# Kernel tuning notes

Measured on AMD Instinct MI355X. Metric: run time of the kernel, lower is better.

## Reference

```python
import jax, jax.numpy as jnp
import numpy as np

B, N, DIM = 1, 32768, 512
HEADS, DIM_HEAD, AGENT_NUM = 8, 64, 256
INNER = HEADS * DIM_HEAD  # 512 == DIM
SCALE = DIM_HEAD ** -0.5


def setup_inputs() -> dict:
    key = jax.random.key(0)
    ks = jax.random.split(key, 9)
    s = lambda fan: 1.0 / np.sqrt(fan)
    return {
        "x": jax.random.normal(ks[0], (B, N, DIM), dtype=jnp.float32),
        "W_qkv": jax.random.normal(ks[1], (3 * INNER, DIM), dtype=jnp.float32) * s(DIM),
        "agent": jax.random.normal(ks[2], (HEADS, AGENT_NUM, DIM_HEAD), dtype=jnp.float32),
        "W_noise": jax.random.normal(ks[3], (DIM_HEAD, DIM_HEAD), dtype=jnp.float32) * s(DIM_HEAD),
        "b_noise": jax.random.normal(ks[4], (DIM_HEAD,), dtype=jnp.float32) * s(DIM_HEAD),
        "W_mask": jax.random.normal(ks[5], (DIM_HEAD, DIM_HEAD), dtype=jnp.float32) * s(DIM_HEAD),
        "b_mask": jax.random.normal(ks[6], (DIM_HEAD,), dtype=jnp.float32) * s(DIM_HEAD),
        "W_thresh": jax.random.normal(ks[7], (1, DIM), dtype=jnp.float32) * s(DIM),
        "b_thresh": jax.random.normal(ks[8], (1,), dtype=jnp.float32) * s(DIM),
    }


def reference(x, W_qkv, agent, W_noise, b_noise, W_mask, b_mask, W_thresh, b_thresh):
    b, n, _ = x.shape
    h, d, a = HEADS, DIM_HEAD, AGENT_NUM
    # qkv projection (no bias), split and reshape to b h n d
    qkv = x @ W_qkv.T                                  # [b, n, 3*h*d]
    q, k, v = jnp.split(qkv, 3, axis=-1)
    tohd = lambda t: t.reshape(b, n, h, d).transpose(0, 2, 1, 3)  # [b,h,n,d]
    q, k, v = tohd(q), tohd(k), tohd(v)
    # agent attention: q attends to agents, agents attend to k
    q_attn = jax.nn.softmax(jnp.einsum('bhnd,had->bhna', q, agent) * SCALE, axis=-1)  # [b,h,n,a]
    k_attn = jax.nn.softmax(jnp.einsum('had,bhnd->bhan', agent, k), axis=-1)          # [b,h,a,n]
    kv = jnp.einsum('bhan,bhnd->bhad', k_attn, v)      # [b,h,a,d]
    # threshold from pooled kv (classical): Linear(dim,1) -> mean -> sigmoid
    kv_c = kv.reshape(b, a, h * d)                     # row-major reshape, same as torch
    thresh = jax.nn.sigmoid(jnp.mean(kv_c @ W_thresh.T + b_thresh))
    # noise / mask gating
    noise = jax.nn.sigmoid(kv @ W_noise.T + b_noise)
    mask_v = jax.nn.sigmoid(kv @ W_mask.T + b_mask)
    mask_b = jnp.where(mask_v > thresh, 1.0, 0.0).astype(kv.dtype)
    kv = kv * mask_b + noise                           # tem == 0
    kv = jax.nn.softmax(kv, axis=-1)
    out = jnp.einsum('bhna,bhad->bhnd', q_attn, kv)    # [b,h,n,d]
    return out.transpose(0, 2, 1, 3).reshape(b, n, h * d)
```

## Files before the change

### kernel.cpp

```cpp
#include <hip/hip_runtime.h>
#include <hip/hip_bf16.h>
#include <math.h>

#define N_TOK 32768
#define DIMX 512
#define HEADS 8
#define DHEAD 64
#define ANUM 256
#define SCALE_Q 0.125f
#define KVCHUNK 1024
#define NCHUNK 32
#define STRIP 8192

typedef __bf16 v8bf __attribute__((ext_vector_type(8)));
typedef float v4f __attribute__((ext_vector_type(4)));
typedef unsigned short u16x8 __attribute__((ext_vector_type(8)));

typedef __attribute__((address_space(1))) const void gas_void;
typedef __attribute__((address_space(3))) void las_void;

__device__ __forceinline__ void gld16(const void* g, void* l) {
    __builtin_amdgcn_global_load_lds((gas_void*)g, (las_void*)l, 16, 0, 0);
}

__device__ inline unsigned short f2bf(float f) {
    unsigned u = __float_as_uint(f);
    return (unsigned short)((u + 0x7fffu + ((u >> 16) & 1u)) >> 16);
}
__device__ inline float bf2f(unsigned short s) {
    return __uint_as_float((unsigned)s << 16);
}

__global__ __launch_bounds__(256) void k_cvt3(const float* __restrict__ src,
                                              unsigned short* __restrict__ ph,
                                              unsigned short* __restrict__ pm,
                                              unsigned short* __restrict__ pl,
                                              int n8) {
    for (int i = blockIdx.x * 256 + threadIdx.x; i < n8; i += gridDim.x * 256) {
        float4 a = ((const float4*)src)[2 * i];
        float4 b = ((const float4*)src)[2 * i + 1];
        float v[8] = {a.x, a.y, a.z, a.w, b.x, b.y, b.z, b.w};
        u16x8 H, M, L;
        #pragma unroll
        for (int j = 0; j < 8; ++j) {
            unsigned short h = f2bf(v[j]);
            float r1 = v[j] - bf2f(h);
            unsigned short m = f2bf(r1);
            float r2 = r1 - bf2f(m);
            H[j] = h; M[j] = m; L[j] = f2bf(r2);
        }
        ((u16x8*)ph)[i] = H;
        ((u16x8*)pm)[i] = M;
        ((u16x8*)pl)[i] = L;
    }
}

__global__ __launch_bounds__(256, 2) void k_gemm(
        const unsigned short* __restrict__ xh, const unsigned short* __restrict__ xm,
        const unsigned short* __restrict__ xl,
        const unsigned short* __restrict__ wh, const unsigned short* __restrict__ wm,
        const unsigned short* __restrict__ wl,
        unsigned short* __restrict__ qb, float* __restrict__ kvb,
        unsigned short* __restrict__ vhg, unsigned short* __restrict__ vmg, int mbase) {
    __shared__ __align__(16) unsigned short lds[6 * 4096];
    unsigned short* Ah = lds;
    unsigned short* Am = lds + 4096;
    unsigned short* Al = lds + 8192;
    unsigned short* Bh = lds + 12288;
    unsigned short* Bm = lds + 16384;
    unsigned short* Bl = lds + 20480;
    const int tid = threadIdx.x;
    const int lane = tid & 63;
    const int wid = tid >> 6;
    const int wr = wid >> 1;
    const int wc = wid & 1;
    const int lin = blockIdx.x;
    const int swz = (lin & 7) * 96 + (lin >> 3);
    const int mloc0 = (swz / 12) * 128;
    const int j0 = (swz % 12) * 128;
    const bool isQ = (j0 < 512);
#define SWZ(row, ks) ((row) * 64 + (((ks) ^ (((row) >> 1) & 3)) << 4))
    const int srow0 = tid >> 2;
    const int srow1 = srow0 + 64;
    const int ksw = tid & 3;
    const int ks0 = ksw ^ ((srow0 >> 1) & 3);
    const int ks1 = ksw ^ ((srow1 >> 1) & 3);
    const size_t ga0 = (size_t)(mloc0 + srow0) * DIMX + ks0 * 8;
    const size_t ga1 = (size_t)(mloc0 + srow1) * DIMX + ks1 * 8;
    const size_t gb0 = (size_t)(j0 + srow0) * DIMX + ks0 * 8;
    const size_t gb1 = (size_t)(j0 + srow1) * DIMX + ks1 * 8;
    const int lo0 = tid * 16;
    const int lo1 = 4096 + tid * 16;

    v4f acc[4][4];
    #pragma unroll
    for (int i = 0; i < 4; ++i)
        #pragma unroll
        for (int j = 0; j < 4; ++j)
            #pragma unroll
            for (int r = 0; r < 4; ++r) acc[i][j][r] = 0.0f;

    const int fm = lane & 15;
    const int fks = lane >> 4;
    int aofs[4], bofs[4];
    #pragma unroll
    for (int i = 0; i < 4; ++i) {
        const int am = wr * 64 + i * 16 + fm;
        const int bm = wc * 64 + i * 16 + fm;
        aofs[i] = SWZ(am, fks);
        bofs[i] = SWZ(bm, fks);
    }
#undef SWZ

    for (int k0 = 0; k0 < DIMX; k0 += 32) {
        __syncthreads();
        gld16(xh + ga0 + k0, (char*)Ah + lo0);
        gld16(xh + ga1 + k0, (char*)Ah + lo1);
        gld16(xm + ga0 + k0, (char*)Am + lo0);
        gld16(xm + ga1 + k0, (char*)Am + lo1);
        gld16(wh + gb0 + k0, (char*)Bh + lo0);
        gld16(wh + gb1 + k0, (char*)Bh + lo1);
        gld16(wm + gb0 + k0, (char*)Bm + lo0);
        gld16(wm + gb1 + k0, (char*)Bm + lo1);
        if (!isQ) {
            gld16(xl + ga0 + k0, (char*)Al + lo0);
            gld16(xl + ga1 + k0, (char*)Al + lo1);
            gld16(wl + gb0 + k0, (char*)Bl + lo0);
            gld16(wl + gb1 + k0, (char*)Bl + lo1);
        }
        __syncthreads();
        v8bf fah[4], fbh[4];
        #pragma unroll
        for (int i = 0; i < 4; ++i) {
            fah[i] = *(const v8bf*)((const char*)Ah + aofs[i]);
            fbh[i] = *(const v8bf*)((const char*)Bh + bofs[i]);
        }
        #pragma unroll
        for (int mi = 0; mi < 4; ++mi)
            #pragma unroll
            for (int ni = 0; ni < 4; ++ni)
                acc[mi][ni] = __builtin_amdgcn_mfma_f32_16x16x32_bf16(fah[mi], fbh[ni], acc[mi][ni], 0, 0, 0);
        v8bf fam[4], fbm[4];
        #pragma unroll
        for (int i = 0; i < 4; ++i) {
            fam[i] = *(const v8bf*)((const char*)Am + aofs[i]);
            fbm[i] = *(const v8bf*)((const char*)Bm + bofs[i]);
        }
        #pragma unroll
        for (int mi = 0; mi < 4; ++mi)
            #pragma unroll
            for (int ni = 0; ni < 4; ++ni) {
                acc[mi][ni] = __builtin_amdgcn_mfma_f32_16x16x32_bf16(fah[mi], fbm[ni], acc[mi][ni], 0, 0, 0);
                acc[mi][ni] = __builtin_amdgcn_mfma_f32_16x16x32_bf16(fam[mi], fbh[ni], acc[mi][ni], 0, 0, 0);
            }
        if (!isQ) {
            #pragma unroll
            for (int mi = 0; mi < 4; ++mi)
                #pragma unroll
                for (int ni = 0; ni < 4; ++ni)
                    acc[mi][ni] = __builtin_amdgcn_mfma_f32_16x16x32_bf16(fam[mi], fbm[ni], acc[mi][ni], 0, 0, 0);
            v8bf fal[4], fbl[4];
            #pragma unroll
            for (int i = 0; i < 4; ++i) {
                fal[i] = *(const v8bf*)((const char*)Al + aofs[i]);
                fbl[i] = *(const v8bf*)((const char*)Bl + bofs[i]);
            }
            #pragma unroll
            for (int mi = 0; mi < 4; ++mi)
                #pragma unroll
                for (int ni = 0; ni < 4; ++ni) {
                    acc[mi][ni] = __builtin_amdgcn_mfma_f32_16x16x32_bf16(fah[mi], fbl[ni], acc[mi][ni], 0, 0, 0);
                    acc[mi][ni] = __builtin_amdgcn_mfma_f32_16x16x32_bf16(fal[mi], fbh[ni], acc[mi][ni], 0, 0, 0);
                }
        }
    }
    const int crow = (lane >> 4) * 4;
    const int ccol = lane & 15;
    if (isQ) {
        #pragma unroll
        for (int mi = 0; mi < 4; ++mi)
            #pragma unroll
            for (int ni = 0; ni < 4; ++ni) {
                const int j = j0 + wc * 64 + ni * 16 + ccol;
                #pragma unroll
                for (int r = 0; r < 4; ++r) {
                    const int m = mbase + mloc0 + wr * 64 + mi * 16 + crow + r;
                    qb[(size_t)m * DIMX + j] = f2bf(acc[mi][ni][r]);
                }
            }
    } else if (j0 < 1024) {
        #pragma unroll
        for (int mi = 0; mi < 4; ++mi)
            #pragma unroll
            for (int ni = 0; ni < 4; ++ni) {
                const int j = j0 - 512 + wc * 64 + ni * 16 + ccol;
                #pragma unroll
                for (int r = 0; r < 4; ++r) {
                    const int m = mbase + mloc0 + wr * 64 + mi * 16 + crow + r;
                    kvb[(size_t)m * 512 + j] = acc[mi][ni][r];
                }
            }
    } else {
        #pragma unroll
        for (int mi = 0; mi < 4; ++mi)
            #pragma unroll
            for (int ni = 0; ni < 4; ++ni) {
                const int j = j0 - 1024 + wc * 64 + ni * 16 + ccol;
                #pragma unroll
                for (int r = 0; r < 4; ++r) {
                    const int m = mbase + mloc0 + wr * 64 + mi * 16 + crow + r;
                    const float val = acc[mi][ni][r];
                    const unsigned short hb = f2bf(val);
                    vhg[(size_t)m * 512 + j] = hb;
                    vmg[(size_t)m * 512 + j] = f2bf(val - bf2f(hb));
                }
            }
    }
}

__global__ __launch_bounds__(512, 1) void k_kvagg(
        const float* __restrict__ kvb,
        const unsigned short* __restrict__ vhg, const unsigned short* __restrict__ vmg,
        const unsigned short* __restrict__ agh, const unsigned short* __restrict__ agm,
        const unsigned short* __restrict__ agl,
        float* __restrict__ pacc, float* __restrict__ psum) {
    __shared__ __align__(16) char S[61440];
    const int h = blockIdx.x, chunk = blockIdx.y;
    const int t = threadIdx.x, lane = t & 63, w = t >> 6;
    const int fr = lane & 15, fc = lane >> 4;
    const int n0 = chunk * KVCHUNK;
    v8bf agf[3][2][2];
    #pragma unroll
    for (int mt = 0; mt < 2; ++mt)
        #pragma unroll
        for (int ks = 0; ks < 2; ++ks) {
            const size_t ix = ((size_t)(h * ANUM + w * 32 + mt * 16 + fr)) * 64 + ks * 32 + fc * 8;
            agf[0][mt][ks] = *(const v8bf*)(agh + ix);
            agf[1][mt][ks] = *(const v8bf*)(agm + ix);
            agf[2][mt][ks] = *(const v8bf*)(agl + ix);
        }
    const int cn = t >> 4;
    const int cd0 = (t & 15) * 4;
    float4 kreg; ushort4 vhr, vmr;
    {
        const size_t gix = ((size_t)(n0 + cn)) * 512 + h * 64 + cd0;
        kreg = *(const float4*)(kvb + gix);
        vhr = *(const ushort4*)(vhg + gix);
        vmr = *(const ushort4*)(vmg + gix);
    }
    v4f kvacc[2][4];
    #pragma unroll
    for (int mt = 0; mt < 2; ++mt)
        #pragma unroll
        for (int nt = 0; nt < 4; ++nt)
            #pragma unroll
            for (int r = 0; r < 4; ++r) kvacc[mt][nt][r] = 0.f;
    float sacc[2][4] = {{0.f,0.f,0.f,0.f},{0.f,0.f,0.f,0.f}};

    for (int it = 0; it < 32; ++it) {
        __syncthreads();
        {
            ushort4 H, M, L;
            unsigned short hh;
            hh = f2bf(kreg.x); { float r1 = kreg.x - bf2f(hh); M.x = f2bf(r1);
                L.x = f2bf(r1 - bf2f(M.x)); H.x = hh; }
            hh = f2bf(kreg.y); { float r1 = kreg.y - bf2f(hh); M.y = f2bf(r1);
                L.y = f2bf(r1 - bf2f(M.y)); H.y = hh; }
            hh = f2bf(kreg.z); { float r1 = kreg.z - bf2f(hh); M.z = f2bf(r1);
                L.z = f2bf(r1 - bf2f(M.z)); H.z = hh; }
            hh = f2bf(kreg.w); { float r1 = kreg.w - bf2f(hh); M.w = f2bf(r1);
                L.w = f2bf(r1 - bf2f(M.w)); H.w = hh; }
            const int kb0 = cn * 128 + ((cd0 * 2) ^ ((cn & 7) << 4));
            *(ushort4*)(S + kb0) = H;
            *(ushort4*)(S + 4096 + kb0) = M;
            *(ushort4*)(S + 8192 + kb0) = L;
            const unsigned short vh4[4] = {vhr.x, vhr.y, vhr.z, vhr.w};
            const unsigned short vm4[4] = {vmr.x, vmr.y, vmr.z, vmr.w};
            #pragma unroll
            for (int i = 0; i < 4; ++i) {
                const int d = cd0 + i;
                const int vb = d * 128 + ((cn * 2) ^ ((d & 7) << 4));
                *(unsigned short*)(S + 12288 + vb) = vh4[i];
                *(unsigned short*)(S + 20480 + vb) = vm4[i];
            }
        }
        if (it < 31) {
            const size_t gix = ((size_t)(n0 + (it + 1) * 32 + cn)) * 512 + h * 64 + cd0;
            kreg = *(const float4*)(kvb + gix);
            vhr = *(const ushort4*)(vhg + gix);
            vmr = *(const ushort4*)(vmg + gix);
        }
        __syncthreads();
        v4f C[2][2];
        #pragma unroll
        for (int mt = 0; mt < 2; ++mt)
            #pragma unroll
            for (int nt = 0; nt < 2; ++nt)
                #pragma unroll
                for (int r = 0; r < 4; ++r) C[mt][nt][r] = 0.f;
        #pragma unroll
        for (int ks = 0; ks < 2; ++ks) {
            v8bf kb[3][2];
            #pragma unroll
            for (int nt = 0; nt < 2; ++nt) {
                const int row = nt * 16 + fr;
                const int off = row * 128 + ((ks * 64 + fc * 16) ^ ((row & 7) << 4));
                kb[0][nt] = *(const v8bf*)(S + off);
                kb[1][nt] = *(const v8bf*)(S + 4096 + off);
                kb[2][nt] = *(const v8bf*)(S + 8192 + off);
            }
            #pragma unroll
            for (int mt = 0; mt < 2; ++mt)
                #pragma unroll
                for (int nt = 0; nt < 2; ++nt) {
                    C[mt][nt] = __builtin_amdgcn_mfma_f32_16x16x32_bf16(agf[0][mt][ks], kb[0][nt], C[mt][nt], 0, 0, 0);
                    C[mt][nt] = __builtin_amdgcn_mfma_f32_16x16x32_bf16(agf[0][mt][ks], kb[1][nt], C[mt][nt], 0, 0, 0);
                    C[mt][nt] = __builtin_amdgcn_mfma_f32_16x16x32_bf16(agf[1][mt][ks], kb[0][nt], C[mt][nt], 0, 0, 0);
                    C[mt][nt] = __builtin_amdgcn_mfma_f32_16x16x32_bf16(agf[1][mt][ks], kb[1][nt], C[mt][nt], 0, 0, 0);
                    C[mt][nt] = __builtin_amdgcn_mfma_f32_16x16x32_bf16(agf[0][mt][ks], kb[2][nt], C[mt][nt], 0, 0, 0);
                    C[mt][nt] = __builtin_amdgcn_mfma_f32_16x16x32_bf16(agf[2][mt][ks], kb[0][nt], C[mt][nt], 0, 0, 0);
                }
        }
        const int pbase = 28672 + w * 4096;
        #pragma unroll
        for (int mt = 0; mt < 2; ++mt) {
            float sl[4] = {0.f, 0.f, 0.f, 0.f};
            #pragma unroll
            for (int nt = 0; nt < 2; ++nt)
                #pragma unroll
                for (int r = 0; r < 4; ++r) {
                    const float pv = __expf(C[mt][nt][r] - 20.f);
                    sl[r] += pv;
                    const unsigned short ph = f2bf(pv);
                    const unsigned short pmv = f2bf(pv - bf2f(ph));
                    const int a = mt * 16 + fc * 4 + r;
                    const int off = pbase + a * 64 + (((nt * 16 + fr) * 2) ^ ((a & 3) << 4));
                    *(unsigned short*)(S + off) = ph;
                    *(unsigned short*)(S + off + 2048) = pmv;
                }
            #pragma unroll
            for (int r = 0; r < 4; ++r) {
                float v = sl[r];
                v += __shfl_xor(v, 1, 64); v += __shfl_xor(v, 2, 64);
                v += __shfl_xor(v, 4, 64); v += __shfl_xor(v, 8, 64);
                sacc[mt][r] += v;
            }
        }
        v8bf pah[2], pam[2];
        #pragma unroll
        for (int mt = 0; mt < 2; ++mt) {
            const int a = mt * 16 + fr;
            const int off = pbase + a * 64 + ((fc * 16) ^ ((a & 3) << 4));
            pah[mt] = *(const v8bf*)(S + off);
            pam[mt] = *(const v8bf*)(S + off + 2048);
        }
        #pragma unroll
        for (int nt = 0; nt < 4; ++nt) {
            const int d = nt * 16 + fr;
            const int off = 12288 + d * 128 + ((fc * 16) ^ ((d & 7) << 4));
            v8bf vbh = *(const v8bf*)(S + off);
            v8bf vbm = *(const v8bf*)(S + off + 8192);
            #pragma unroll
            for (int mt = 0; mt < 2; ++mt) {
                kvacc[mt][nt] = __builtin_amdgcn_mfma_f32_16x16x32_bf16(pah[mt], vbh, kvacc[mt][nt], 0, 0, 0);
                kvacc[mt][nt] = __builtin_amdgcn_mfma_f32_16x16x32_bf16(pah[mt], vbm, kvacc[mt][nt], 0, 0, 0);
                kvacc[mt][nt] = __builtin_amdgcn_mfma_f32_16x16x32_bf16(pam[mt], vbh, kvacc[mt][nt], 0, 0, 0);
                kvacc[mt][nt] = __builtin_amdgcn_mfma_f32_16x16x32_bf16(pam[mt], vbm, kvacc[mt][nt], 0, 0, 0);
            }
        }
    }
    const size_t base = (size_t)chunk * HEADS + h;
    #pragma unroll
    for (int mt = 0; mt < 2; ++mt)
        #pragma unroll
        for (int r = 0; r < 4; ++r)
            if (fr == 0)
                psum[base * ANUM + w * 32 + mt * 16 + fc * 4 + r] = sacc[mt][r];
    #pragma unroll
    for (int mt = 0; mt < 2; ++mt)
        #pragma unroll
        for (int nt = 0; nt < 4; ++nt)
            #pragma unroll
            for (int r = 0; r < 4; ++r)
                pacc[base * (ANUM * DHEAD) +
                     (size_t)(w * 32 + mt * 16 + fc * 4 + r) * 64 + nt * 16 + fr] =
                    kvacc[mt][nt][r];
}

__global__ __launch_bounds__(256) void k_combine(const float* __restrict__ pacc,
                                                 const float* __restrict__ psum,
                                                 float* __restrict__ kv) {
    const int idx = blockIdx.x * 256 + threadIdx.x;
    const int ha = idx >> 6;
    float a = 0.f, s = 0.f;
    for (int c = 0; c < NCHUNK; ++c) {
        a += pacc[(size_t)c*131072 + idx];
        s += psum[c*2048 + ha];
    }
    kv[idx] = a / s;
}

__global__ __launch_bounds__(256) void k_thresh_part(const float* __restrict__ kv,
                                                     const float* __restrict__ Wt,
                                                     float* __restrict__ part) {
    __shared__ float red[256];
    const int t = threadIdx.x;
    const int base = blockIdx.x * 1024 + t * 4;
    float4 kvv = *(const float4*)&kv[base];
    float4 wv  = *(const float4*)&Wt[base & (DIMX - 1)];
    red[t] = kvv.x * wv.x + kvv.y * wv.y + kvv.z * wv.z + kvv.w * wv.w;
    __syncthreads();
    for (int off = 128; off > 0; off >>= 1) {
        if (t < off) red[t] += red[t + off];
        __syncthreads();
    }
    if (t == 0) part[blockIdx.x] = red[0];
}

__global__ __launch_bounds__(128) void k_thresh_fin(const float* __restrict__ part,
                                                    const float* __restrict__ bt,
                                                    float* __restrict__ th) {
    __shared__ float red[128];
    const int t = threadIdx.x;
    red[t] = part[t];
    __syncthreads();
    for (int off = 64; off > 0; off >>= 1) {
        if (t < off) red[t] += red[t + off];
        __syncthreads();
    }
    if (t == 0) {
        float m = red[0] / (float)ANUM + bt[0];
        th[0] = 1.f / (1.f + expf(-m));
    }
}

__global__ __launch_bounds__(64) void k_gate(const float* __restrict__ kv,
                                             const float* __restrict__ Wn,
                                             const float* __restrict__ bn,
                                             const float* __restrict__ Wm,
                                             const float* __restrict__ bm,
                                             const float* __restrict__ th,
                                             unsigned short* __restrict__ kth,
                                             unsigned short* __restrict__ ktm) {
    const int rowi = blockIdx.x;
    const int d = threadIdx.x;
    __shared__ __align__(16) float r[64];
    r[d] = kv[(size_t)rowi*64 + d];
    __syncthreads();
    float sn = bn[d], sm = bm[d];
    #pragma unroll
    for (int j4 = 0; j4 < 16; ++j4) {
        float4 rr = *(const float4*)&r[j4*4];
        float4 w1 = *(const float4*)&Wn[d*64 + j4*4];
        float4 w2 = *(const float4*)&Wm[d*64 + j4*4];
        sn += rr.x*w1.x + rr.y*w1.y + rr.z*w1.z + rr.w*w1.w;
        sm += rr.x*w2.x + rr.y*w2.y + rr.z*w2.z + rr.w*w2.w;
    }
    float noise = 1.f/(1.f + __expf(-sn));
    float maskv = 1.f/(1.f + __expf(-sm));
    float tval = th[0];
    float val = r[d] * (maskv > tval ? 1.f : 0.f) + noise;
    float m = val;
    #pragma unroll
    for (int off = 32; off > 0; off >>= 1) m = fmaxf(m, __shfl_xor(m, off, 64));
    float e = __expf(val - m);
    float ssum = e;
    #pragma unroll
    for (int off = 32; off > 0; off >>= 1) ssum += __shfl_xor(ssum, off, 64);
    const float res = e / ssum;
    const int hh = rowi >> 8;
    const int a  = rowi & 255;
    unsigned short hb = f2bf(res);
    const size_t tix = ((size_t)hh * DHEAD + d) * ANUM + a;
    kth[tix] = hb;
    ktm[tix] = f2bf(res - bf2f(hb));
}

__global__ __launch_bounds__(256, 4) void k_out_mfma(
        const unsigned short* __restrict__ qb,
        const unsigned short* __restrict__ agh, const unsigned short* __restrict__ agm,
        const unsigned short* __restrict__ kth, const unsigned short* __restrict__ ktm,
        float* __restrict__ out) {
    __shared__ __align__(16) unsigned short P[64 * 256];
    __shared__ float s_red[4][64];
    const int t = threadIdx.x;
    const int lane = t & 63;
    const int w = t >> 6;
    const int h = blockIdx.y;
    const int n0 = blockIdx.x * 64;
    const int fr = lane & 15;
    const int fc = lane >> 4;
    v8bf qa[4][2];
    #pragma unroll
    for (int mt = 0; mt < 4; ++mt) {
        const unsigned short* qp = qb + (size_t)(n0 + mt * 16 + fr) * DIMX + h * DHEAD + fc * 8;
        qa[mt][0] = *(const v8bf*)qp;
        qa[mt][1] = *(const v8bf*)(qp + 32);
    }
    v4f C[4][4];
    #pragma unroll
    for (int i = 0; i < 4; ++i)
        #pragma unroll
        for (int j = 0; j < 4; ++j)
            #pragma unroll
            for (int r = 0; r < 4; ++r) C[i][j][r] = 0.f;
    const int a0w = w * 64;
    __builtin_amdgcn_s_setprio(1);
    #pragma unroll
    for (int nt = 0; nt < 4; ++nt) {
        const size_t bix = ((size_t)h * ANUM + a0w + nt * 16 + fr) * DHEAD + fc * 8;
        v8bf B0h = *(const v8bf*)(agh + bix);
        v8bf B1h = *(const v8bf*)(agh + bix + 32);
        v8bf B0m = *(const v8bf*)(agm + bix);
        v8bf B1m = *(const v8bf*)(agm + bix + 32);
        #pragma unroll
        for (int mt = 0; mt < 4; ++mt) {
            C[mt][nt] = __builtin_amdgcn_mfma_f32_16x16x32_bf16(qa[mt][0], B0h, C[mt][nt], 0, 0, 0);
            C[mt][nt] = __builtin_amdgcn_mfma_f32_16x16x32_bf16(qa[mt][1], B1h, C[mt][nt], 0, 0, 0);
            C[mt][nt] = __builtin_amdgcn_mfma_f32_16x16x32_bf16(qa[mt][0], B0m, C[mt][nt], 0, 0, 0);
            C[mt][nt] = __builtin_amdgcn_mfma_f32_16x16x32_bf16(qa[mt][1], B1m, C[mt][nt], 0, 0, 0);
        }
    }
    __builtin_amdgcn_s_setprio(0);
    #pragma unroll
    for (int mt = 0; mt < 4; ++mt)
        #pragma unroll
        for (int r = 0; r < 4; ++r) {
            const int tok = mt * 16 + fc * 4 + r;
            const int sw = (tok & 7) << 4;
            float pv[4];
            float sloc = 0.f;
            #pragma unroll
            for (int nt = 0; nt < 4; ++nt) {
                pv[nt] = __expf(C[mt][nt][r] * SCALE_Q);
                sloc += pv[nt];
            }
            #pragma unroll
            for (int m = 1; m < 16; m <<= 1) sloc += __shfl_xor(sloc, m, 64);
            if (fr == 0) s_red[w][tok] = sloc;
            #pragma unroll
            for (int nt = 0; nt < 4; ++nt) {
                const int ag = a0w + nt * 16 + fr;
                *(unsigned short*)((char*)P + ((tok * 512 + ag * 2) ^ sw)) = f2bf(pv[nt]);
            }
        }
    __syncthreads();
    v4f D[4];
    #pragma unroll
    for (int tg = 0; tg < 4; ++tg)
        #pragma unroll
        for (int r = 0; r < 4; ++r) D[tg][r] = 0.f;
    const int dcol = w * 16 + fr;
    __builtin_amdgcn_s_setprio(1);
    #pragma unroll
    for (int ks = 0; ks < 8; ++ks) {
        const size_t bix = ((size_t)h * DHEAD + dcol) * ANUM + fc * 8 + ks * 32;
        v8bf vh = *(const v8bf*)(kth + bix);
        v8bf vm = *(const v8bf*)(ktm + bix);
        #pragma unroll
        for (int tg = 0; tg < 4; ++tg) {
            const int tok = tg * 16 + fr;
            const int sw = (tok & 7) << 4;
            v8bf pa = *(const v8bf*)((const char*)P + ((tok * 512 + fc * 16 + ks * 64) ^ sw));
            D[tg] = __builtin_amdgcn_mfma_f32_16x16x32_bf16(pa, vh, D[tg], 0, 0, 0);
            D[tg] = __builtin_amdgcn_mfma_f32_16x16x32_bf16(pa, vm, D[tg], 0, 0, 0);
        }
    }
    __builtin_amdgcn_s_setprio(0);
    #pragma unroll
    for (int tg = 0; tg < 4; ++tg)
        #pragma unroll
        for (int r = 0; r < 4; ++r) {
            const int tok = tg * 16 + fc * 4 + r;
            const float inv = 1.f / (s_red[0][tok] + s_red[1][tok] + s_red[2][tok] + s_red[3][tok]);
            out[(size_t)(n0 + tok) * DIMX + h * DHEAD + dcol] = D[tg][r] * inv;
        }
}

extern "C" void kernel_launch(void* const* d_in, const int* in_sizes, int n_in,
                              void* d_out, int out_size, void* d_ws, size_t ws_size,
                              hipStream_t stream) {
    const float* x     = (const float*)d_in[0];
    const float* Wqkv  = (const float*)d_in[1];
    const float* agent = (const float*)d_in[2];
    const float* Wn    = (const float*)d_in[3];
    const float* bn    = (const float*)d_in[4];
    const float* Wm    = (const float*)d_in[5];
    const float* bm    = (const float*)d_in[6];
    const float* Wt    = (const float*)d_in[7];
    const float* bt    = (const float*)d_in[8];
    float* out = (float*)d_out;

    const size_t KB_F  = (size_t)N_TOK * 512;
    const size_t VB_E  = (size_t)N_TOK * 512;
    const size_t QB_E  = (size_t)N_TOK * DIMX;
    const size_t WSP_E = (size_t)3 * DIMX * DIMX;
    const size_t XSP_E = (size_t)STRIP * DIMX;
    const size_t PACC_F = (size_t)NCHUNK * HEADS * ANUM * DHEAD;
    const size_t PSUM_F = (size_t)NCHUNK * HEADS * ANUM;
    const size_t KV_F   = (size_t)HEADS * ANUM * DHEAD;

    char* p = (char*)d_ws;
    float* kvb = (float*)p;            p += KB_F * 4;
    unsigned short* vhg = (unsigned short*)p;  p += VB_E * 2;
    unsigned short* vmg = (unsigned short*)p;  p += VB_E * 2;
    unsigned short* qbuf = (unsigned short*)p; p += QB_E * 2;
    unsigned short* wh = (unsigned short*)p;   p += WSP_E * 2;
    unsigned short* wm = (unsigned short*)p;   p += WSP_E * 2;
    unsigned short* wl = (unsigned short*)p;   p += WSP_E * 2;
    unsigned short* xh = (unsigned short*)p;   p += XSP_E * 2;
    unsigned short* xm = (unsigned short*)p;   p += XSP_E * 2;
    unsigned short* xl = (unsigned short*)p;   p += XSP_E * 2;
    float* pacc = (float*)p;           p += PACC_F * 4;
    float* psum = (float*)p;           p += PSUM_F * 4;
    float* kv   = (float*)p;           p += KV_F * 4;
    unsigned short* agh = (unsigned short*)p;  p += KV_F * 2;
    unsigned short* agm = (unsigned short*)p;  p += KV_F * 2;
    unsigned short* agl = (unsigned short*)p;  p += KV_F * 2;
    unsigned short* kth = (unsigned short*)p;  p += KV_F * 2;
    unsigned short* ktm = (unsigned short*)p;  p += KV_F * 2;
    float* th   = (float*)p;           p += 64;
    float* thpart = (float*)p;         p += 128 * 4;
    if (ws_size < (size_t)(p - (char*)d_ws)) return;

    k_cvt3<<<384, 256, 0, stream>>>(Wqkv, wh, wm, wl, (int)(WSP_E / 8));
    k_cvt3<<<64, 256, 0, stream>>>(agent, agh, agm, agl, (int)(KV_F / 8));
    for (int s = 0; s < N_TOK / STRIP; ++s) {
        k_cvt3<<<2048, 256, 0, stream>>>(x + (size_t)s * STRIP * DIMX, xh, xm, xl,
                                         (int)(XSP_E / 8));
        k_gemm<<<768, 256, 0, stream>>>(xh, xm, xl, wh, wm, wl,
                                        qbuf, kvb, vhg, vmg, s * STRIP);
    }
    k_kvagg <<<dim3(HEADS, NCHUNK), 512, 0, stream>>>(kvb, vhg, vmg, agh, agm, agl,
                                                      pacc, psum);
    k_combine<<<512, 256, 0, stream>>>(pacc, psum, kv);
    k_thresh_part<<<128, 256, 0, stream>>>(kv, Wt, thpart);
    k_thresh_fin<<<1, 128, 0, stream>>>(thpart, bt, th);
    k_gate  <<<HEADS*ANUM, 64, 0, stream>>>(kv, Wn, bn, Wm, bm, th, kth, ktm);
    k_out_mfma<<<dim3(N_TOK/64, HEADS), 256, 0, stream>>>(qbuf, agh, agm, kth, ktm, out);
}
```

Measured before the change: 500.9 us.

## Halve kv-aggregation chunk size, raise occupancy, widen P-tile swizzle, alias workspace

Splits the token dimension of the k-attention/kv aggregation into 64 chunks of 512 instead of 32 of 1024, doubling the grid of k_kvagg. Its launch bounds now ask for up to 4 blocks per CU instead of 1. The per-wave P staging area in LDS is re-laid out so the high and low halves of each row sit in one 128-byte row, with a new swizzle meant to reduce bank conflicts. The x split buffers and the partial accumulators now share workspace memory, which is safe because they are used in separate phases. The cost is twice as much partial data for k_combine to read and reduce, and possible register pressure from the tighter launch bound.

```diff
diff --git a/kernel.cpp b/kernel.cpp
--- a/kernel.cpp
+++ b/kernel.cpp
@@ -8,8 +8,8 @@
 #define DHEAD 64
 #define ANUM 256
 #define SCALE_Q 0.125f
-#define KVCHUNK 1024
-#define NCHUNK 32
+#define KVCHUNK 512
+#define NCHUNK 64
 #define STRIP 8192
 
 typedef __bf16 v8bf __attribute__((ext_vector_type(8)));
@@ -218,7 +218,8 @@
     }
 }
 
-__global__ __launch_bounds__(512, 1) void k_kvagg(
+#define PSWZ(a) ((((a) & 3) << 4) | ((((a) >> 2) & 1) << 6))
+__global__ __launch_bounds__(512, 4) void k_kvagg(
         const float* __restrict__ kvb,
         const unsigned short* __restrict__ vhg, const unsigned short* __restrict__ vmg,
         const unsigned short* __restrict__ agh, const unsigned short* __restrict__ agm,
@@ -257,7 +258,7 @@
             for (int r = 0; r < 4; ++r) kvacc[mt][nt][r] = 0.f;
     float sacc[2][4] = {{0.f,0.f,0.f,0.f},{0.f,0.f,0.f,0.f}};
 
-    for (int it = 0; it < 32; ++it) {
+    for (int it = 0; it < KVCHUNK / 32; ++it) {
         __syncthreads();
         {
             ushort4 H, M, L;
@@ -284,7 +285,7 @@
                 *(unsigned short*)(S + 20480 + vb) = vm4[i];
             }
         }
-        if (it < 31) {
+        if (it < KVCHUNK / 32 - 1) {
             const size_t gix = ((size_t)(n0 + (it + 1) * 32 + cn)) * 512 + h * 64 + cd0;
             kreg = *(const float4*)(kvb + gix);
             vhr = *(const ushort4*)(vhg + gix);
@@ -334,9 +335,9 @@
                     const unsigned short ph = f2bf(pv);
                     const unsigned short pmv = f2bf(pv - bf2f(ph));
                     const int a = mt * 16 + fc * 4 + r;
-                    const int off = pbase + a * 64 + (((nt * 16 + fr) * 2) ^ ((a & 3) << 4));
-                    *(unsigned short*)(S + off) = ph;
-                    *(unsigned short*)(S + off + 2048) = pmv;
+                    const int cb = (nt * 16 + fr) * 2;
+                    *(unsigned short*)(S + pbase + a * 128 + (cb ^ PSWZ(a))) = ph;
+                    *(unsigned short*)(S + pbase + a * 128 + ((cb + 64) ^ PSWZ(a))) = pmv;
                 }
             #pragma unroll
             for (int r = 0; r < 4; ++r) {
@@ -350,9 +351,8 @@
         #pragma unroll
         for (int mt = 0; mt < 2; ++mt) {
             const int a = mt * 16 + fr;
-            const int off = pbase + a * 64 + ((fc * 16) ^ ((a & 3) << 4));
-            pah[mt] = *(const v8bf*)(S + off);
-            pam[mt] = *(const v8bf*)(S + off + 2048);
+            pah[mt] = *(const v8bf*)(S + pbase + a * 128 + ((fc * 16) ^ PSWZ(a)));
+            pam[mt] = *(const v8bf*)(S + pbase + a * 128 + ((fc * 16 + 64) ^ PSWZ(a)));
         }
         #pragma unroll
         for (int nt = 0; nt < 4; ++nt) {
@@ -386,6 +386,7 @@
                      (size_t)(w * 32 + mt * 16 + fc * 4 + r) * 64 + nt * 16 + fr] =
                     kvacc[mt][nt][r];
 }
+#undef PSWZ
 
 __global__ __launch_bounds__(256) void k_combine(const float* __restrict__ pacc,
                                                  const float* __restrict__ psum,
@@ -608,11 +609,17 @@
     unsigned short* wh = (unsigned short*)p;   p += WSP_E * 2;
     unsigned short* wm = (unsigned short*)p;   p += WSP_E * 2;
     unsigned short* wl = (unsigned short*)p;   p += WSP_E * 2;
-    unsigned short* xh = (unsigned short*)p;   p += XSP_E * 2;
-    unsigned short* xm = (unsigned short*)p;   p += XSP_E * 2;
-    unsigned short* xl = (unsigned short*)p;   p += XSP_E * 2;
-    float* pacc = (float*)p;           p += PACC_F * 4;
-    float* psum = (float*)p;           p += PSUM_F * 4;
+    char* ubase = p;
+    unsigned short* xh = (unsigned short*)ubase;
+    unsigned short* xm = xh + XSP_E;
+    unsigned short* xl = xm + XSP_E;
+    float* pacc = (float*)ubase;
+    float* psum = (float*)(ubase + PACC_F * 4);
+    {
+        const size_t xsz = 3 * XSP_E * 2;
+        const size_t psz = PACC_F * 4 + PSUM_F * 4;
+        p = ubase + (xsz > psz ? xsz : psz);
+    }
     float* kv   = (float*)p;           p += KV_F * 4;
     unsigned short* agh = (unsigned short*)p;  p += KV_F * 2;
     unsigned short* agm = (unsigned short*)p;  p += KV_F * 2;
```

New measurement: 593.6 us. +18.5%, slower.
